# Optimization experiments

Hardware: AMD Instinct MI355X
Metric: run time of the kernel (lower is better)

## Reference

```python
import jax, jax.numpy as jnp
import numpy as np

EMBED_DIM = 2048
HEAD_DIM = 128
B, T = 4, 2048


def setup_inputs() -> dict:
    key = jax.random.key(0)
    k1, k2, k3, k4 = jax.random.split(key, 4)
    x_in = jax.random.normal(k1, (B, T, EMBED_DIM), dtype=jnp.float32)
    scale = 1.0 / np.sqrt(EMBED_DIM)
    Wq = jax.random.normal(k2, (EMBED_DIM, HEAD_DIM), dtype=jnp.float32) * scale
    Wk = jax.random.normal(k3, (EMBED_DIM, HEAD_DIM), dtype=jnp.float32) * scale
    Wv = jax.random.normal(k4, (EMBED_DIM, HEAD_DIM), dtype=jnp.float32) * scale
    return {"x_in": x_in, "Wq": Wq, "Wk": Wk, "Wv": Wv}


def reference(x_in, Wq, Wk, Wv):
    # x_in: [B, T, E]; projections (Linear, no bias)
    q = jnp.einsum('bte,ed->btd', x_in, Wq)  # [B,T,D]
    k = jnp.einsum('bte,ed->btd', x_in, Wk)
    v = jnp.einsum('bte,ed->btd', x_in, Wv)
    t = x_in.shape[1]
    d = Wq.shape[1]
    s = jnp.einsum('btd,bsd->bts', q, k) / jnp.sqrt(jnp.asarray(d, q.dtype))  # [B,Tq,Tk]
    # causal mask: positions with tril==0 (k index > q index) -> -inf
    causal = jnp.tril(jnp.ones((t, t), dtype=bool))
    s = jnp.where(causal, s, -jnp.inf)
    # NOTE: original module applies softmax over dim=1 (query axis), faithfully reproduced
    a = jax.nn.softmax(s, axis=1)
    z = jnp.einsum('bts,bsd->btd', a, v)  # [B,T,D]
    return z
```

## Files before the change

kernel.cpp:

```cpp
#include <hip/hip_runtime.h>

typedef _Float16 f16x8 __attribute__((ext_vector_type(8)));
typedef _Float16 f16x4 __attribute__((ext_vector_type(4)));
typedef float f32x4 __attribute__((ext_vector_type(4)));

#define T_DIM 2048
#define E_DIM 2048
#define D_DIM 128
#define NB 4
#define KSP_P 8
#define KCH_P 256
#define KSP_A 8
#define KCH_A 256

__device__ __forceinline__ void gll16(const void* g, void* l) {
  __builtin_amdgcn_global_load_lds(
      (const __attribute__((address_space(1))) unsigned int*)g,
      (__attribute__((address_space(3))) unsigned int*)l, 16, 0, 0);
}


__global__ void prep(const float* __restrict__ Wq, const float* __restrict__ Wk,
                     const float* __restrict__ Wv, _Float16* __restrict__ WhT,
                     float* __restrict__ Z, float* __restrict__ L) {
  int idx = blockIdx.x * 256 + threadIdx.x;
  int y = blockIdx.y;
  if (y < 3) {
    const float* W = (y == 0) ? Wq : ((y == 1) ? Wk : Wv);
    int e = idx & (E_DIM - 1), d = idx >> 11;
    WhT[(size_t)y * (D_DIM * E_DIM) + idx] = (_Float16)W[e * D_DIM + d];
  } else {
    f32x4 z = {0.f, 0.f, 0.f, 0.f};
    *(f32x4*)(Z + (size_t)idx * 4) = z;
    if (idx < NB * T_DIM) L[idx] = 0.f;
  }
}


__global__ __launch_bounds__(768) void proj_gemm(
    const float* __restrict__ x, const _Float16* __restrict__ WhT,
    _Float16* __restrict__ Ph) {
  __shared__ _Float16 A16[2][128 * 32];
  __shared__ _Float16 Bsw[2][384 * 32];
  const int tid = threadIdx.x, w = tid >> 6, lane = tid & 63;
  const int wn = w >> 1, wr = w & 1, quad = lane >> 4, l16 = lane & 15;
  const int t0 = blockIdx.x * 128;
  const int ks = blockIdx.y;
  const int kb = ks * KCH_P;
  const int arowA = tid >> 2, asegA = tid & 3;
  const int aswA = (asegA ^ ((arowA >> 1) & 3)) * 8;
  const int br = tid >> 2, bseg = tid & 3;

  f32x4 ax0, ax1;
  auto loadA = [&](int k0) {
    if (tid < 512) {
      const float* src = x + (size_t)(t0 + arowA) * E_DIM + k0 + asegA * 8;
      ax0 = *(const f32x4*)src;
      ax1 = *(const f32x4*)(src + 4);
    }
  };
  auto writeA = [&](int buf) {
    if (tid < 512) {
      f16x8 o;
#pragma unroll
      for (int e = 0; e < 4; ++e) {
        o[e] = (_Float16)ax0[e];
        o[e + 4] = (_Float16)ax1[e];
      }
      *(f16x8*)(&A16[buf][arowA * 32 + aswA]) = o;
    }
  };
  auto stageB = [&](int buf, int k0) {
    int g = bseg ^ ((br >> 1) & 3);
    gll16(WhT + (size_t)br * E_DIM + k0 + g * 8, &Bsw[buf][br * 32 + bseg * 8]);
    int r = 192 + br;
    int g2 = bseg ^ ((r >> 1) & 3);
    gll16(WhT + (size_t)r * E_DIM + k0 + g2 * 8, &Bsw[buf][r * 32 + bseg * 8]);
  };

  f32x4 acc[4][4] = {};
  loadA(kb);
  stageB(0, kb);
  asm volatile("s_waitcnt vmcnt(0)" ::: "memory");
  writeA(0);
  const int NIT = KCH_P / 32;
  for (int it = 0; it < NIT; ++it) {
    const int cur = it & 1;
    __syncthreads();
    if (it + 1 < NIT) {
      loadA(kb + (it + 1) * 32);
      stageB(cur ^ 1, kb + (it + 1) * 32);
    }
    f16x8 af[4], bf[4];
#pragma unroll
    for (int i = 0; i < 4; ++i) {
      int row = wr * 64 + i * 16 + l16;
      int sg = (quad ^ ((row >> 1) & 3)) * 8;
      af[i] = *(const f16x8*)(&A16[cur][row * 32 + sg]);
    }
#pragma unroll
    for (int j = 0; j < 4; ++j) {
      int row = wn * 64 + j * 16 + l16;
      int sg = (quad ^ ((row >> 1) & 3)) * 8;
      bf[j] = *(const f16x8*)(&Bsw[cur][row * 32 + sg]);
    }
    __builtin_amdgcn_s_setprio(1);
#pragma unroll
    for (int i = 0; i < 4; ++i)
#pragma unroll
      for (int j = 0; j < 4; ++j)
        acc[i][j] = __builtin_amdgcn_mfma_f32_16x16x32_f16(af[i], bf[j], acc[i][j], 0, 0, 0);
    __builtin_amdgcn_s_setprio(0);
    if (it + 1 < NIT) {
      asm volatile("s_waitcnt vmcnt(0)" ::: "memory");
      writeA(cur ^ 1);
    }
  }
  const int mat = wn >> 1;
  const int nb0 = (wn & 1) * 64;
  _Float16* P = Ph + ((size_t)(ks * 3 + mat) << 20);
  if (mat < 2) {
#pragma unroll
    for (int i = 0; i < 4; ++i)
#pragma unroll
      for (int j = 0; j < 4; ++j) {
        int n = nb0 + j * 16 + l16;
#pragma unroll
        for (int r = 0; r < 4; ++r) {
          int t = t0 + wr * 64 + i * 16 + quad * 4 + r;
          P[(size_t)t * D_DIM + n] = (_Float16)acc[i][j][r];
        }
      }
  } else {
#pragma unroll
    for (int i = 0; i < 4; ++i)
#pragma unroll
      for (int j = 0; j < 4; ++j) {
        int n = nb0 + j * 16 + l16;
        int t = t0 + wr * 64 + i * 16 + quad * 4;
        f16x4 o;
#pragma unroll
        for (int r = 0; r < 4; ++r) o[r] = (_Float16)acc[i][j][r];
        *(f16x4*)(P + ((size_t)(t >> 11) * D_DIM + n) * T_DIM + (t & (T_DIM - 1))) = o;
      }
  }
}


__global__ void proj_reduce(const _Float16* __restrict__ Ph, _Float16* __restrict__ Qh,
                            _Float16* __restrict__ Kh, _Float16* __restrict__ VT) {
  size_t u = ((size_t)blockIdx.x * 256 + threadIdx.x) * 8;
  int mat = (int)(u >> 20);
  size_t rem = u & ((1u << 20) - 1);
  float s[8] = {};
#pragma unroll
  for (int ks = 0; ks < KSP_P; ++ks) {
    f16x8 p = *(const f16x8*)(Ph + ((size_t)(ks * 3 + mat) << 20) + rem);
#pragma unroll
    for (int e = 0; e < 8; ++e) s[e] += (float)p[e];
  }
  f16x8 o;
#pragma unroll
  for (int e = 0; e < 8; ++e) o[e] = (_Float16)s[e];
  _Float16* dst = (mat == 0) ? Qh : ((mat == 1) ? Kh : VT);
  *(f16x8*)(dst + rem) = o;
}


__global__ __launch_bounds__(256) void s_gemm(const _Float16* __restrict__ Qh,
                                              const _Float16* __restrict__ Kh,
                                              _Float16* __restrict__ S,
                                              float* __restrict__ L) {
  int idx = blockIdx.x;
  int xt = (int)((sqrtf(8.f * idx + 1.f) - 1.f) * 0.5f);
  while ((xt + 1) * (xt + 2) / 2 <= idx) ++xt;
  while (xt * (xt + 1) / 2 > idx) --xt;
  int yt = idx - xt * (xt + 1) / 2;
  __shared__ _Float16 Bs[4][128 * 32];
  const int tid = threadIdx.x, w = tid >> 6, lane = tid & 63;
  const int wr = w >> 1, wc = w & 1, quad = lane >> 4, l16 = lane & 15;
  const int t0 = xt * 128, s0 = yt * 128, b = blockIdx.y;
  const _Float16* A = Qh + (size_t)b * T_DIM * D_DIM;
  const _Float16* B = Kh + (size_t)b * T_DIM * D_DIM;
  const int srow = lane >> 2;
  const int swz = ((lane & 3) ^ ((srow >> 1) & 3)) * 8;
#pragma unroll
  for (int kq = 0; kq < 4; ++kq)
#pragma unroll
    for (int q = 0; q < 2; ++q) {
      int rbase = w * 32 + q * 16;
      gll16(B + (size_t)(s0 + rbase + srow) * D_DIM + kq * 32 + swz,
            Bs[kq] + rbase * 32);
    }
  __syncthreads();
  f32x4 acc[4][4] = {};
  const int bsg = (quad ^ ((l16 >> 1) & 3)) * 8;
#pragma unroll
  for (int kq = 0; kq < 4; ++kq) {
    f16x8 af[4], bf[4];
#pragma unroll
    for (int i = 0; i < 4; ++i)
      af[i] = *(const f16x8*)(A + (size_t)(t0 + wr * 64 + i * 16 + l16) * D_DIM +
                              kq * 32 + quad * 8);
#pragma unroll
    for (int j = 0; j < 4; ++j)
      bf[j] = *(const f16x8*)(Bs[kq] + (wc * 64 + j * 16 + l16) * 32 + bsg);
#pragma unroll
    for (int i = 0; i < 4; ++i)
#pragma unroll
      for (int j = 0; j < 4; ++j)
        acc[i][j] = __builtin_amdgcn_mfma_f32_16x16x32_f16(af[i], bf[j], acc[i][j], 0, 0, 0);
  }
  _Float16* Sb = S + (size_t)b * T_DIM * T_DIM;
  const float scale = 0.08838834764831845f;
#pragma unroll
  for (int j = 0; j < 4; ++j) {
    const int s = s0 + wc * 64 + j * 16 + l16;
    float l = 0.f;
#pragma unroll
    for (int i = 0; i < 4; ++i)
#pragma unroll
      for (int r = 0; r < 4; ++r) {
        int t = t0 + wr * 64 + i * 16 + quad * 4 + r;
        float e = (s > t) ? 0.f : __expf(acc[i][j][r] * scale);
        Sb[(size_t)t * T_DIM + s] = (_Float16)e;
        l += e;
      }
    l += __shfl_xor(l, 16, 64);
    l += __shfl_xor(l, 32, 64);
    if (quad == 0) atomicAdd(&L[(size_t)b * T_DIM + s], l);
  }
}


__global__ __launch_bounds__(256) void av_gemm(const _Float16* __restrict__ S,
                                               const _Float16* __restrict__ VT,
                                               const float* __restrict__ L,
                                               float* __restrict__ Z) {
  const int t0 = blockIdx.x * 128, b = blockIdx.y, ks = blockIdx.z;
  const int Kmax = t0 + 128;
  const int Kstart = ks * KCH_A;
  if (Kstart >= Kmax) return;
  const int Kend = (Kstart + KCH_A < Kmax) ? (Kstart + KCH_A) : Kmax;
  const int nit = (Kend - Kstart) >> 5;
  __shared__ _Float16 As[2][128 * 32];
  __shared__ _Float16 Bs[2][128 * 32];
  __shared__ float Ls[KCH_A];
  const int tid = threadIdx.x, w = tid >> 6, lane = tid & 63;
  const int wr = w >> 1, wc = w & 1, quad = lane >> 4, l16 = lane & 15;
  const _Float16* Sb = S + (size_t)b * T_DIM * T_DIM;
  const _Float16* Vb = VT + (size_t)b * D_DIM * T_DIM;
  for (int i = tid; i < Kend - Kstart; i += 256)
    Ls[i] = 1.f / L[b * T_DIM + Kstart + i];
  const int srow = lane >> 2;
  const int arow = tid >> 2, aseg = tid & 3;
  const int asw = (aseg ^ ((arow >> 1) & 3)) * 8;
  f16x8 sv0, sv1;
  auto loadS = [&](int k0) {
    sv0 = *(const f16x8*)(Sb + (size_t)(t0 + arow) * T_DIM + k0 + aseg * 8);
    sv1 = *(const f16x8*)(Sb + (size_t)(t0 + 64 + arow) * T_DIM + k0 + aseg * 8);
  };
  auto stageB = [&](int buf, int k0) {
#pragma unroll
    for (int q = 0; q < 2; ++q) {
      int rbase = w * 32 + q * 16;
      int row = rbase + srow;
      int g = ((lane & 3) ^ ((row >> 1) & 3)) * 8;
      gll16(Vb + (size_t)row * T_DIM + k0 + g, Bs[buf] + rbase * 32);
    }
  };
  auto writeA = [&](int buf, int k0) {
#pragma unroll
    for (int q = 0; q < 2; ++q) {
      f16x8 v = q ? sv1 : sv0;
      f16x8 o;
#pragma unroll
      for (int e = 0; e < 8; ++e) {
        int li = k0 + aseg * 8 + e - Kstart;
        o[e] = (_Float16)((float)v[e] * Ls[li]);
      }
      *(f16x8*)(As[buf] + (q * 64 + arow) * 32 + asw) = o;
    }
  };
  f32x4 acc[4][4] = {};
  __syncthreads();
  loadS(Kstart);
  stageB(0, Kstart);
  asm volatile("s_waitcnt vmcnt(0)" ::: "memory");
  writeA(0, Kstart);
  for (int it = 0; it < nit; ++it) {
    const int cur = it & 1;
    const int k0 = Kstart + it * 32;
    __syncthreads();
    if (it + 1 < nit) {
      loadS(k0 + 32);
      stageB(cur ^ 1, k0 + 32);
    }
    f16x8 af[4], bf[4];
#pragma unroll
    for (int i = 0; i < 4; ++i) {
      int row = wr * 64 + i * 16 + l16;
      int sg = (quad ^ ((row >> 1) & 3)) * 8;
      af[i] = *(const f16x8*)(As[cur] + row * 32 + sg);
    }
#pragma unroll
    for (int j = 0; j < 4; ++j) {
      int row = wc * 64 + j * 16 + l16;
      int sg = (quad ^ ((row >> 1) & 3)) * 8;
      bf[j] = *(const f16x8*)(Bs[cur] + row * 32 + sg);
    }
    __builtin_amdgcn_s_setprio(1);
#pragma unroll
    for (int i = 0; i < 4; ++i)
#pragma unroll
      for (int j = 0; j < 4; ++j)
        acc[i][j] = __builtin_amdgcn_mfma_f32_16x16x32_f16(af[i], bf[j], acc[i][j], 0, 0, 0);
    __builtin_amdgcn_s_setprio(0);
    if (it + 1 < nit) {
      asm volatile("s_waitcnt vmcnt(0)" ::: "memory");
      writeA(cur ^ 1, k0 + 32);
    }
  }
  float* Zb = Z + (size_t)b * T_DIM * D_DIM;
#pragma unroll
  for (int i = 0; i < 4; ++i)
#pragma unroll
    for (int j = 0; j < 4; ++j) {
      int n = wc * 64 + j * 16 + l16;
#pragma unroll
      for (int r = 0; r < 4; ++r) {
        int t = t0 + wr * 64 + i * 16 + quad * 4 + r;
        atomicAdd(&Zb[(size_t)t * D_DIM + n], acc[i][j][r]);
      }
    }
}


extern "C" void kernel_launch(void* const* d_in, const int* in_sizes, int n_in,
                              void* d_out, int out_size, void* d_ws, size_t ws_size,
                              hipStream_t stream) {
  const float* x = (const float*)d_in[0];
  const float* Wq = (const float*)d_in[1];
  const float* Wk = (const float*)d_in[2];
  const float* Wv = (const float*)d_in[3];
  char* ws = (char*)d_ws;
  _Float16* Ph = (_Float16*)(ws);
  _Float16* S = (_Float16*)(ws);
  _Float16* WhT = (_Float16*)(ws + 50331648);
  _Float16* Qh = (_Float16*)(ws + 51904512);
  _Float16* Kh = (_Float16*)(ws + 54001664);
  _Float16* VT = (_Float16*)(ws + 56098816);
  float* L = (float*)(ws + 58195968);
  float* Z = (float*)d_out;

  prep<<<dim3(1024, 4), 256, 0, stream>>>(Wq, Wk, Wv, WhT, Z, L);
  proj_gemm<<<dim3(64, KSP_P), 768, 0, stream>>>(x, WhT, Ph);
  proj_reduce<<<1536, 256, 0, stream>>>(Ph, Qh, Kh, VT);
  s_gemm<<<dim3(136, 4), 256, 0, stream>>>(Qh, Kh, S, L);
  av_gemm<<<dim3(16, 4, KSP_A), 256, 0, stream>>>(S, VT, L, Z);
}
```

Baseline: 173.1 us.

## Halve projection split-K and double the K tile per iteration to 64

The projection GEMM now splits K into 4 chunks of 512 instead of 8 chunks of 256, and each loop iteration stages a 64-wide K slice with an 8-way XOR swizzle instead of a 32-wide slice. This halves the fp16 partial buffer that proj_reduce must write and read, and halves the number of barrier-separated iterations relative to MFMA work. In exchange, LDS use per block doubles to about 128 KB and the grid drops to 256 blocks, so there is roughly one block per CU and less latency hiding. Workspace offsets shrink to match the smaller partial buffer.

After: 161.6 us. 1.07x faster.

```diff
diff --git a/kernel.cpp b/kernel.cpp
--- a/kernel.cpp
+++ b/kernel.cpp
@@ -8,8 +8,8 @@
 #define E_DIM 2048
 #define D_DIM 128
 #define NB 4
-#define KSP_P 8
-#define KCH_P 256
+#define KSP_P 4
+#define KCH_P 512
 #define KSP_A 8
 #define KCH_A 256
 
@@ -40,42 +40,49 @@
 __global__ __launch_bounds__(768) void proj_gemm(
     const float* __restrict__ x, const _Float16* __restrict__ WhT,
     _Float16* __restrict__ Ph) {
-  __shared__ _Float16 A16[2][128 * 32];
-  __shared__ _Float16 Bsw[2][384 * 32];
+  __shared__ _Float16 A16[2][128 * 64];
+  __shared__ _Float16 Bsw[2][384 * 64];
   const int tid = threadIdx.x, w = tid >> 6, lane = tid & 63;
   const int wn = w >> 1, wr = w & 1, quad = lane >> 4, l16 = lane & 15;
   const int t0 = blockIdx.x * 128;
   const int ks = blockIdx.y;
   const int kb = ks * KCH_P;
-  const int arowA = tid >> 2, asegA = tid & 3;
-  const int aswA = (asegA ^ ((arowA >> 1) & 3)) * 8;
-  const int br = tid >> 2, bseg = tid & 3;
-
-  f32x4 ax0, ax1;
+  const int arow = tid >> 2, ac16 = (tid & 3) * 16;
+  const int as0 = ((tid & 3) * 2) ^ (arow & 7);
+  const int as1 = ((tid & 3) * 2 + 1) ^ (arow & 7);
+
+  f32x4 ax0, ax1, ax2, ax3;
   auto loadA = [&](int k0) {
     if (tid < 512) {
-      const float* src = x + (size_t)(t0 + arowA) * E_DIM + k0 + asegA * 8;
+      const float* src = x + (size_t)(t0 + arow) * E_DIM + k0 + ac16;
       ax0 = *(const f32x4*)src;
       ax1 = *(const f32x4*)(src + 4);
+      ax2 = *(const f32x4*)(src + 8);
+      ax3 = *(const f32x4*)(src + 12);
     }
   };
   auto writeA = [&](int buf) {
     if (tid < 512) {
-      f16x8 o;
+      f16x8 o0, o1;
 #pragma unroll
       for (int e = 0; e < 4; ++e) {
-        o[e] = (_Float16)ax0[e];
-        o[e + 4] = (_Float16)ax1[e];
-      }
-      *(f16x8*)(&A16[buf][arowA * 32 + aswA]) = o;
+        o0[e] = (_Float16)ax0[e];
+        o0[e + 4] = (_Float16)ax1[e];
+        o1[e] = (_Float16)ax2[e];
+        o1[e + 4] = (_Float16)ax3[e];
+      }
+      *(f16x8*)(&A16[buf][arow * 64 + as0 * 8]) = o0;
+      *(f16x8*)(&A16[buf][arow * 64 + as1 * 8]) = o1;
     }
   };
   auto stageB = [&](int buf, int k0) {
-    int g = bseg ^ ((br >> 1) & 3);
-    gll16(WhT + (size_t)br * E_DIM + k0 + g * 8, &Bsw[buf][br * 32 + bseg * 8]);
-    int r = 192 + br;
-    int g2 = bseg ^ ((r >> 1) & 3);
-    gll16(WhT + (size_t)r * E_DIM + k0 + g2 * 8, &Bsw[buf][r * 32 + bseg * 8]);
+#pragma unroll
+    for (int p = 0; p < 4; ++p) {
+      int item = p * 768 + tid;
+      int row = item >> 3, seg = item & 7;
+      int g = seg ^ (row & 7);
+      gll16(WhT + (size_t)row * E_DIM + k0 + g * 8, &Bsw[buf][item * 8]);
+    }
   };
 
   f32x4 acc[4][4] = {};
@@ -83,33 +90,36 @@
   stageB(0, kb);
   asm volatile("s_waitcnt vmcnt(0)" ::: "memory");
   writeA(0);
-  const int NIT = KCH_P / 32;
+  const int NIT = KCH_P / 64;
   for (int it = 0; it < NIT; ++it) {
     const int cur = it & 1;
     __syncthreads();
     if (it + 1 < NIT) {
-      loadA(kb + (it + 1) * 32);
-      stageB(cur ^ 1, kb + (it + 1) * 32);
-    }
-    f16x8 af[4], bf[4];
-#pragma unroll
-    for (int i = 0; i < 4; ++i) {
-      int row = wr * 64 + i * 16 + l16;
-      int sg = (quad ^ ((row >> 1) & 3)) * 8;
-      af[i] = *(const f16x8*)(&A16[cur][row * 32 + sg]);
-    }
-#pragma unroll
-    for (int j = 0; j < 4; ++j) {
-      int row = wn * 64 + j * 16 + l16;
-      int sg = (quad ^ ((row >> 1) & 3)) * 8;
-      bf[j] = *(const f16x8*)(&Bsw[cur][row * 32 + sg]);
+      loadA(kb + (it + 1) * 64);
+      stageB(cur ^ 1, kb + (it + 1) * 64);
     }
     __builtin_amdgcn_s_setprio(1);
 #pragma unroll
-    for (int i = 0; i < 4; ++i)
-#pragma unroll
-      for (int j = 0; j < 4; ++j)
-        acc[i][j] = __builtin_amdgcn_mfma_f32_16x16x32_f16(af[i], bf[j], acc[i][j], 0, 0, 0);
+    for (int kq = 0; kq < 2; ++kq) {
+      f16x8 af[4], bf[4];
+#pragma unroll
+      for (int i = 0; i < 4; ++i) {
+        int row = wr * 64 + i * 16 + l16;
+        int sg = ((kq * 4 + quad) ^ (row & 7)) * 8;
+        af[i] = *(const f16x8*)(&A16[cur][row * 64 + sg]);
+      }
+#pragma unroll
+      for (int j = 0; j < 4; ++j) {
+        int row = wn * 64 + j * 16 + l16;
+        int sg = ((kq * 4 + quad) ^ (row & 7)) * 8;
+        bf[j] = *(const f16x8*)(&Bsw[cur][row * 64 + sg]);
+      }
+#pragma unroll
+      for (int i = 0; i < 4; ++i)
+#pragma unroll
+        for (int j = 0; j < 4; ++j)
+          acc[i][j] = __builtin_amdgcn_mfma_f32_16x16x32_f16(af[i], bf[j], acc[i][j], 0, 0, 0);
+    }
     __builtin_amdgcn_s_setprio(0);
     if (it + 1 < NIT) {
       asm volatile("s_waitcnt vmcnt(0)" ::: "memory");
@@ -346,11 +356,11 @@
   char* ws = (char*)d_ws;
   _Float16* Ph = (_Float16*)(ws);
   _Float16* S = (_Float16*)(ws);
-  _Float16* WhT = (_Float16*)(ws + 50331648);
-  _Float16* Qh = (_Float16*)(ws + 51904512);
-  _Float16* Kh = (_Float16*)(ws + 54001664);
-  _Float16* VT = (_Float16*)(ws + 56098816);
-  float* L = (float*)(ws + 58195968);
+  _Float16* WhT = (_Float16*)(ws + 33554432);
+  _Float16* Qh = (_Float16*)(ws + 35127296);
+  _Float16* Kh = (_Float16*)(ws + 37224448);
+  _Float16* VT = (_Float16*)(ws + 39321600);
+  float* L = (float*)(ws + 41418752);
   float* Z = (float*)d_out;
 
   prep<<<dim3(1024, 4), 256, 0, stream>>>(Wq, Wk, Wv, WhT, Z, L);
```

## Triple-buffer projection GEMM, halve its K split, stage Q tiles in LDS

Applied to the files above, without the earlier changes.

The projection GEMM now runs 4 K-splits of 512 instead of 8 of 256. Its main loop becomes a 3-stage LDS ring with prefetch distance 2, using partial vmcnt waits and raw s_barrier in place of a full drain and __syncthreads. The S GEMM also stages Q tiles into LDS through global_load_lds instead of reading A fragments straight from global memory, and workspace offsets shrink to match the smaller partial buffer. This is meant to hide load latency, cut reduction traffic, and get coalesced A loads, at the cost of more LDS per block, fewer blocks in the projection grid, and fragile hand-tuned waitcnt counts.

Measured after the change: 160.1 us. -7.5%, faster.

```diff
diff --git a/kernel.cpp b/kernel.cpp
--- a/kernel.cpp
+++ b/kernel.cpp
@@ -8,8 +8,8 @@
 #define E_DIM 2048
 #define D_DIM 128
 #define NB 4
-#define KSP_P 8
-#define KCH_P 256
+#define KSP_P 4
+#define KCH_P 512
 #define KSP_A 8
 #define KCH_A 256
 
@@ -40,34 +40,41 @@
 __global__ __launch_bounds__(768) void proj_gemm(
     const float* __restrict__ x, const _Float16* __restrict__ WhT,
     _Float16* __restrict__ Ph) {
-  __shared__ _Float16 A16[2][128 * 32];
-  __shared__ _Float16 Bsw[2][384 * 32];
+  __shared__ _Float16 A16[3][128 * 32];
+  __shared__ _Float16 Bsw[3][384 * 32];
   const int tid = threadIdx.x, w = tid >> 6, lane = tid & 63;
   const int wn = w >> 1, wr = w & 1, quad = lane >> 4, l16 = lane & 15;
   const int t0 = blockIdx.x * 128;
   const int ks = blockIdx.y;
   const int kb = ks * KCH_P;
-  const int arowA = tid >> 2, asegA = tid & 3;
-  const int aswA = (asegA ^ ((arowA >> 1) & 3)) * 8;
+  const int arow = tid >> 2, aseg = tid & 3;
+  const int asw = (aseg ^ ((arow >> 1) & 3)) * 8;
   const int br = tid >> 2, bseg = tid & 3;
 
-  f32x4 ax0, ax1;
-  auto loadA = [&](int k0) {
+  f32x4 a0x0, a0x1, a1x0, a1x1;
+  auto loadA = [&](int set, int k0) {
     if (tid < 512) {
-      const float* src = x + (size_t)(t0 + arowA) * E_DIM + k0 + asegA * 8;
-      ax0 = *(const f32x4*)src;
-      ax1 = *(const f32x4*)(src + 4);
-    }
-  };
-  auto writeA = [&](int buf) {
+      const float* src = x + (size_t)(t0 + arow) * E_DIM + k0 + aseg * 8;
+      if (set == 0) {
+        a0x0 = *(const f32x4*)src;
+        a0x1 = *(const f32x4*)(src + 4);
+      } else {
+        a1x0 = *(const f32x4*)src;
+        a1x1 = *(const f32x4*)(src + 4);
+      }
+    }
+  };
+  auto writeA = [&](int buf, int set) {
     if (tid < 512) {
+      f32x4 lo = (set == 0) ? a0x0 : a1x0;
+      f32x4 hi = (set == 0) ? a0x1 : a1x1;
       f16x8 o;
 #pragma unroll
       for (int e = 0; e < 4; ++e) {
-        o[e] = (_Float16)ax0[e];
-        o[e + 4] = (_Float16)ax1[e];
-      }
-      *(f16x8*)(&A16[buf][arowA * 32 + aswA]) = o;
+        o[e] = (_Float16)lo[e];
+        o[e + 4] = (_Float16)hi[e];
+      }
+      *(f16x8*)(&A16[buf][arow * 32 + asw]) = o;
     }
   };
   auto stageB = [&](int buf, int k0) {
@@ -79,30 +86,42 @@
   };
 
   f32x4 acc[4][4] = {};
-  loadA(kb);
+  const int NIT = KCH_P / 32;
+  loadA(0, kb);
   stageB(0, kb);
-  asm volatile("s_waitcnt vmcnt(0)" ::: "memory");
-  writeA(0);
-  const int NIT = KCH_P / 32;
+  loadA(1, kb + 32);
+  stageB(1, kb + 32);
+  writeA(0, 0);
+#pragma unroll
   for (int it = 0; it < NIT; ++it) {
-    const int cur = it & 1;
-    __syncthreads();
-    if (it + 1 < NIT) {
-      loadA(kb + (it + 1) * 32);
-      stageB(cur ^ 1, kb + (it + 1) * 32);
+    const int buf = it % 3;
+    if (it < NIT - 1) {
+      if (tid < 512)
+        asm volatile("s_waitcnt vmcnt(4) lgkmcnt(0)" ::: "memory");
+      else
+        asm volatile("s_waitcnt vmcnt(2) lgkmcnt(0)" ::: "memory");
+    } else {
+      asm volatile("s_waitcnt vmcnt(0) lgkmcnt(0)" ::: "memory");
+    }
+    __builtin_amdgcn_sched_barrier(0);
+    __builtin_amdgcn_s_barrier();
+    __builtin_amdgcn_sched_barrier(0);
+    if (it + 2 < NIT) {
+      loadA((it + 2) & 1, kb + (it + 2) * 32);
+      stageB((it + 2) % 3, kb + (it + 2) * 32);
     }
     f16x8 af[4], bf[4];
 #pragma unroll
     for (int i = 0; i < 4; ++i) {
       int row = wr * 64 + i * 16 + l16;
       int sg = (quad ^ ((row >> 1) & 3)) * 8;
-      af[i] = *(const f16x8*)(&A16[cur][row * 32 + sg]);
+      af[i] = *(const f16x8*)(&A16[buf][row * 32 + sg]);
     }
 #pragma unroll
     for (int j = 0; j < 4; ++j) {
       int row = wn * 64 + j * 16 + l16;
       int sg = (quad ^ ((row >> 1) & 3)) * 8;
-      bf[j] = *(const f16x8*)(&Bsw[cur][row * 32 + sg]);
+      bf[j] = *(const f16x8*)(&Bsw[buf][row * 32 + sg]);
     }
     __builtin_amdgcn_s_setprio(1);
 #pragma unroll
@@ -111,10 +130,7 @@
       for (int j = 0; j < 4; ++j)
         acc[i][j] = __builtin_amdgcn_mfma_f32_16x16x32_f16(af[i], bf[j], acc[i][j], 0, 0, 0);
     __builtin_amdgcn_s_setprio(0);
-    if (it + 1 < NIT) {
-      asm volatile("s_waitcnt vmcnt(0)" ::: "memory");
-      writeA(cur ^ 1);
-    }
+    if (it + 1 < NIT) writeA((it + 1) % 3, (it + 1) & 1);
   }
   const int mat = wn >> 1;
   const int nb0 = (wn & 1) * 64;
@@ -176,6 +192,7 @@
   while ((xt + 1) * (xt + 2) / 2 <= idx) ++xt;
   while (xt * (xt + 1) / 2 > idx) --xt;
   int yt = idx - xt * (xt + 1) / 2;
+  __shared__ _Float16 As_[4][128 * 32];
   __shared__ _Float16 Bs[4][128 * 32];
   const int tid = threadIdx.x, w = tid >> 6, lane = tid & 63;
   const int wr = w >> 1, wc = w & 1, quad = lane >> 4, l16 = lane & 15;
@@ -189,6 +206,8 @@
 #pragma unroll
     for (int q = 0; q < 2; ++q) {
       int rbase = w * 32 + q * 16;
+      gll16(A + (size_t)(t0 + rbase + srow) * D_DIM + kq * 32 + swz,
+            As_[kq] + rbase * 32);
       gll16(B + (size_t)(s0 + rbase + srow) * D_DIM + kq * 32 + swz,
             Bs[kq] + rbase * 32);
     }
@@ -200,8 +219,7 @@
     f16x8 af[4], bf[4];
 #pragma unroll
     for (int i = 0; i < 4; ++i)
-      af[i] = *(const f16x8*)(A + (size_t)(t0 + wr * 64 + i * 16 + l16) * D_DIM +
-                              kq * 32 + quad * 8);
+      af[i] = *(const f16x8*)(As_[kq] + (wr * 64 + i * 16 + l16) * 32 + bsg);
 #pragma unroll
     for (int j = 0; j < 4; ++j)
       bf[j] = *(const f16x8*)(Bs[kq] + (wc * 64 + j * 16 + l16) * 32 + bsg);
@@ -346,11 +364,11 @@
   char* ws = (char*)d_ws;
   _Float16* Ph = (_Float16*)(ws);
   _Float16* S = (_Float16*)(ws);
-  _Float16* WhT = (_Float16*)(ws + 50331648);
-  _Float16* Qh = (_Float16*)(ws + 51904512);
-  _Float16* Kh = (_Float16*)(ws + 54001664);
-  _Float16* VT = (_Float16*)(ws + 56098816);
-  float* L = (float*)(ws + 58195968);
+  _Float16* WhT = (_Float16*)(ws + 33554432);
+  _Float16* Qh = (_Float16*)(ws + 35127296);
+  _Float16* Kh = (_Float16*)(ws + 37224448);
+  _Float16* VT = (_Float16*)(ws + 39321600);
+  float* L = (float*)(ws + 41418752);
   float* Z = (float*)d_out;
 
   prep<<<dim3(1024, 4), 256, 0, stream>>>(Wq, Wk, Wv, WhT, Z, L);
```
